# Performance work log

Measured on AMD Instinct MI355X. Metric: run time of the kernel, lower is better.

The kernel has to match this reference:

```python
import jax, jax.numpy as jnp
import numpy as np

DN = ('NCHW', 'OIHW', 'NCHW')

def conv2d(x, w, b, stride, pad):
    y = jax.lax.conv_general_dilated(x, w, (stride, stride), [(pad, pad), (pad, pad)], dimension_numbers=DN)
    return y + b[None, :, None, None]

def conv_transpose2d(x, w, b):
    # torch ConvTranspose2d(k=4, stride=2, padding=1): out = (H-1)*2 - 2 + 4 = 2H
    # implemented as input-dilated conv with padding k-1-p = 2 on each side
    y = jax.lax.conv_general_dilated(x, w, (1, 1), [(2, 2), (2, 2)], lhs_dilation=(2, 2), dimension_numbers=DN)
    return y + b[None, :, None, None]

def setup_inputs() -> dict:
    key = jax.random.key(0)
    ks = jax.random.split(key, 8)
    K, D = 512, 128
    x = jax.random.normal(ks[0], (32, 3, 128, 128), jnp.float32)
    ew1 = jax.random.normal(ks[1], (128, 3, 4, 4), jnp.float32) * (1.0 / np.sqrt(3 * 16))
    eb1 = jnp.zeros((128,), jnp.float32)
    ew2 = jax.random.normal(ks[2], (D, 128, 4, 4), jnp.float32) * (1.0 / np.sqrt(128 * 16))
    eb2 = jnp.zeros((D,), jnp.float32)
    E = jax.random.uniform(ks[3], (K, D), jnp.float32, minval=-1.0 / K, maxval=1.0 / K)
    dw1 = jax.random.normal(ks[4], (128, D, 4, 4), jnp.float32) * (1.0 / np.sqrt(D * 16))
    db1 = jnp.zeros((128,), jnp.float32)
    dw2 = jax.random.normal(ks[5], (3, 128, 4, 4), jnp.float32) * (1.0 / np.sqrt(128 * 16))
    db2 = jnp.zeros((3,), jnp.float32)
    return {"x": x, "ew1": ew1, "eb1": eb1, "ew2": ew2, "eb2": eb2, "E": E,
            "dw1": dw1, "db1": db1, "dw2": dw2, "db2": db2}

def reference(x, ew1, eb1, ew2, eb2, E, dw1, db1, dw2, db2):
    # --- encoder: conv stack ---
    h = jax.nn.relu(conv2d(x, ew1, eb1, stride=2, pad=1))       # [B,128,64,64]
    z = conv2d(h, ew2, eb2, stride=2, pad=1)                    # [B,D,32,32] encoder_output
    B, C, H, W = z.shape
    Ze = jnp.transpose(z, (0, 2, 3, 1)).reshape(-1, C)          # [N_e, D], BHWC flattening
    # --- VQ: pairwise sq-dist, argmin, codebook lookup (== one-hot matmul in original) ---
    d = (jnp.sum(Ze * Ze, axis=1, keepdims=True)
         + jnp.sum(E * E, axis=1)
         - 2.0 * jnp.matmul(Ze, E.T))                           # [N_e, K]
    idx = jnp.argmin(d, axis=1)                                 # [N_e]
    Zq = E[idx]                                                 # [N_e, D]
    # faithful to original: Zq_mat.view(encoder_output.shape) with NO permute back
    dec_in = Zq.reshape(B, C, H, W)
    # straight-through estimator
    dec_in = z + jax.lax.stop_gradient(dec_in - z)
    # --- decoder: transposed conv stack ---
    g = jax.nn.relu(conv_transpose2d(dec_in, dw1, db1))         # [B,128,64,64]
    x_recon = jax.nn.sigmoid(conv_transpose2d(g, dw2, db2))     # [B,3,128,128]
    return x_recon
```

## Files before the change

kernel.cpp:

```cpp
#include <hip/hip_runtime.h>
#include <hip/hip_bf16.h>
#include <math.h>


typedef __attribute__((ext_vector_type(8))) short bf16x8;
typedef __attribute__((ext_vector_type(4))) float f32x4;

__device__ __forceinline__ void gload16(const void* g, const void* l) {
    __builtin_amdgcn_global_load_lds(
        (const __attribute__((address_space(1))) void*)g,
        (__attribute__((address_space(3))) void*)l, 16, 0, 0);
}

__device__ __forceinline__ int fragoff(int row, int ks, int lane) {
    return (row << 8) + (((ks << 6) + (lane & 0x30)) ^ ((row & 7) << 4));
}
__device__ __forceinline__ int fragoff64(int row, int ks, int lane) {
    return (row << 7) + (((ks << 6) + (lane & 0x30)) ^ ((row & 7) << 4));
}

__global__ __launch_bounds__(256) void k_init(
    const float* __restrict__ ew1, const float* __restrict__ ew2,
    const float* __restrict__ E,   const float* __restrict__ dw1,
    const float* __restrict__ dw2,
    __hip_bfloat16* __restrict__ hb,  __hip_bfloat16* __restrict__ w2s,
    __hip_bfloat16* __restrict__ w1s, __hip_bfloat16* __restrict__ Eb,
    __hip_bfloat16* __restrict__ w1b, __hip_bfloat16* __restrict__ w2db9,
    __hip_bfloat16* __restrict__ dq,  float* __restrict__ s2)
{
    int bid = blockIdx.x, t = threadIdx.x;
    if (bid < 4160) {
        int tid = bid * 256 + t;
        const int NROW = 32 * 2 * 66 * 128;
        if (tid < NROW) {
            int c = tid & 127;
            int xx = (tid >> 7) % 66;
            int r2 = tid / (66 * 128);
            int yy = (r2 & 1) * 65;
            int n = r2 >> 1;
            hb[((n * 66 + yy) * 66 + xx) * 128 + c] = __float2bfloat16(0.f);
        } else {
            int t2 = tid - NROW;
            int c = t2 & 127;
            int xs = (t2 >> 7) & 1;
            int yy = ((t2 >> 8) & 63) + 1;
            int n = t2 >> 14;
            hb[((n * 66 + yy) * 66 + xs * 65) * 128 + c] = __float2bfloat16(0.f);
        }
    } else if (bid < 5184) {
        int tid = (bid - 4160) * 256 + t;
        int cpos = tid & 127, o = (tid >> 7) & 127, rs = tid >> 14;
        int r = rs >> 2, s = rs & 3;
        int slot = cpos >> 3, e = cpos & 7;
        int csrc = ((slot ^ (o & 7)) << 3) | e;
        w2s[tid] = __float2bfloat16(ew2[((o * 128 + csrc) * 4 + r) * 4 + s]);
    } else if (bid < 6208) {
        int tid = (bid - 5184) * 256 + t;
        int cpos = tid & 127, o = (tid >> 7) & 127, m = tid >> 14;
        int pe = (m >> 3) & 1, qe = (m >> 2) & 1, tt = (m >> 1) & 1, u = m & 1;
        int slot = cpos >> 3, e = cpos & 7;
        int csrc = ((slot ^ (o & 7)) << 3) | e;
        w1s[tid] = __float2bfloat16(dw1[((o * 128 + csrc) * 4 + (pe + 2 * tt)) * 4 + (qe + 2 * u)]);
    } else if (bid < 6464) {
        int tid = (bid - 6208) * 256 + t;
        int cpos = tid & 127, k = tid >> 7;
        int slot = cpos >> 3, e = cpos & 7;
        int csrc = ((slot ^ (k & 7)) << 3) | e;
        Eb[tid] = __float2bfloat16(E[k * 128 + csrc]);
    } else if (bid < 6496) {
        int tid = (bid - 6464) * 256 + t;
        int o = tid >> 6, cpos = tid & 63;
        int slot = cpos >> 3, e = cpos & 7;
        int k = ((slot ^ (o & 7)) << 3) | e;
        float v = 0.f;
        if (k < 48) {
            int c = k >> 4, r = (k >> 2) & 3, s = k & 3;
            v = ew1[((o * 3 + c) * 4 + r) * 4 + s];
        }
        w1b[tid] = __float2bfloat16(v);
    } else if (bid < 6568) {
        int tid = (bid - 6496) * 256 + t;
        int cpos = tid & 127;
        int col = (tid >> 7) & 15;
        int de = tid >> 11;
        int o = col & 3, pq = col >> 2;
        int d = de / 3, e_ = de - d * 3;
        int pe = pq >> 1, qe = pq & 1;
        int tt = d - pe, u = e_ - qe;
        float v = 0.f;
        if (o < 3 && tt >= 0 && tt < 2 && u >= 0 && u < 2) {
            int slot = cpos >> 3, el = cpos & 7;
            int csrc = ((slot ^ (col & 7)) << 3) | el;
            v = dw2[((o * 128 + csrc) * 4 + (pe + 2 * tt)) * 4 + (qe + 2 * u)];
        }
        w2db9[tid] = __float2bfloat16(v);
    } else if (bid < 6570) {
        int k = (bid - 6568) * 256 + t;
        float a = 0.f;
        const float* e = E + k * 128;
        for (int c = 0; c < 128; ++c) a = fmaf(e[c], e[c], a);
        s2[k] = a;
    } else {
        int tid = (bid - 6570) * 256 + t;
        int n = tid / 16896;
        int rem = tid - n * 16896;
        int c = rem & 127;
        int pp = rem >> 7;
        int yy, xx;
        if (pp < 68) { yy = (pp >= 34) ? 33 : 0; xx = pp % 34; }
        else { int q = pp - 68; yy = 1 + (q >> 1); xx = (q & 1) * 33; }
        dq[((n * 34 + yy) * 34 + xx) * 128 + c] = __float2bfloat16(0.f);
    }
}

__global__ __launch_bounds__(256) void k_conv1g(
    const float* __restrict__ x, const __hip_bfloat16* __restrict__ w1b,
    const float* __restrict__ b1, __hip_bfloat16* __restrict__ hb)
{
    __shared__ char smem[32768];
    int t = threadIdx.x, lane = t & 63, w = t >> 6;
    int wr = w >> 1, wc = w & 1;
    int bid0 = blockIdx.x;
    int bid = ((bid0 & 7) << 7) | (bid0 >> 3);
    int posbase = bid << 7;

    #pragma unroll
    for (int i = 0; i < 4; ++i)
        gload16(w1b + ((w * 4 + i) * 512 + lane * 8), &smem[16384 + ((w * 4 + i) << 10)]);

    {
        int row = t >> 1, half = t & 1;
        int rowg = posbase + row;
        int n = rowg >> 12, p = (rowg >> 6) & 63, q = rowg & 63;
        #pragma unroll
        for (int j = 0; j < 4; ++j) {
            int d = half * 4 + j;
            int sct = d ^ (row & 7);
            __hip_bfloat16 hv[8];
            #pragma unroll
            for (int e = 0; e < 8; ++e) {
                int k = sct * 8 + e;
                float v = 0.f;
                if (k < 48) {
                    int c = k >> 4, r = (k >> 2) & 3, s4 = k & 3;
                    int y = 2 * p + r - 1, xx = 2 * q + s4 - 1;
                    if (((unsigned)y < 128u) && ((unsigned)xx < 128u))
                        v = x[((n * 3 + c) * 128 + y) * 128 + xx];
                }
                hv[e] = __float2bfloat16(v);
            }
            *(bf16x8*)&smem[(row << 7) + d * 16] = *(bf16x8*)hv;
        }
    }
    __syncthreads();

    f32x4 acc[4][4];
    #pragma unroll
    for (int mi = 0; mi < 4; ++mi)
        #pragma unroll
        for (int ni = 0; ni < 4; ++ni) acc[mi][ni] = (f32x4){0.f, 0.f, 0.f, 0.f};

    #pragma unroll
    for (int ks = 0; ks < 2; ++ks) {
        bf16x8 av[4], bv[4];
        #pragma unroll
        for (int mi = 0; mi < 4; ++mi)
            av[mi] = *(const bf16x8*)&smem[fragoff64((wr << 6) + (mi << 4) + (lane & 15), ks, lane)];
        #pragma unroll
        for (int ni = 0; ni < 4; ++ni)
            bv[ni] = *(const bf16x8*)&smem[16384 + fragoff64((wc << 6) + (ni << 4) + (lane & 15), ks, lane)];
        #pragma unroll
        for (int mi = 0; mi < 4; ++mi)
            #pragma unroll
            for (int ni = 0; ni < 4; ++ni)
                acc[mi][ni] = __builtin_amdgcn_mfma_f32_16x16x32_bf16(av[mi], bv[ni], acc[mi][ni], 0, 0, 0);
    }

    int rg = (lane >> 4) << 2;
    #pragma unroll
    for (int mi = 0; mi < 4; ++mi)
        #pragma unroll
        for (int ni = 0; ni < 4; ++ni) {
            int o = (wc << 6) + (ni << 4) + (lane & 15);
            float bias = b1[o];
            #pragma unroll
            for (int j = 0; j < 4; ++j) {
                int rowg = posbase + (wr << 6) + (mi << 4) + rg + j;
                int n = rowg >> 12, p = (rowg >> 6) & 63, q = rowg & 63;
                float v = acc[mi][ni][j] + bias;
                v = v > 0.f ? v : 0.f;
                hb[((n * 66 + p + 1) * 66 + q + 1) * 128 + o] = __float2bfloat16(v);
            }
        }
}

__global__ __launch_bounds__(256) void k_conv2(
    const __hip_bfloat16* __restrict__ hb, const __hip_bfloat16* __restrict__ w2s,
    const float* __restrict__ b2, __hip_bfloat16* __restrict__ zb)
{
    __shared__ char smem[49152];
    int t = threadIdx.x, lane = t & 63, w = t >> 6;
    int bid0 = blockIdx.x;
    int bid = ((bid0 & 7) << 6) | (bid0 >> 3);
    int posbase = bid << 6;
    int n = posbase >> 10, p0 = (posbase >> 5) & 31;

    int aoff[4];
    #pragma unroll
    for (int i = 0; i < 4; ++i) {
        int row = (((w << 2) + i) << 2) + (lane >> 4);
        int slot = lane & 15;
        int p = p0 + (row >> 5), q = row & 31;
        int csw = (slot ^ (row & 7)) << 3;
        aoff[i] = (((n * 66 + 2 * p) * 66 + 2 * q) << 7) + csw;
    }

    f32x4 acc[4][2];
    #pragma unroll
    for (int mi = 0; mi < 4; ++mi)
        #pragma unroll
        for (int ni = 0; ni < 2; ++ni) acc[mi][ni] = (f32x4){0.f, 0.f, 0.f, 0.f};

    for (int rs = 0; rs < 16; ++rs) {
        __syncthreads();
        int rsoff = (((rs >> 2) * 66 + (rs & 3)) << 7);
        const __hip_bfloat16* wsl = w2s + (rs << 14);
        #pragma unroll
        for (int i = 0; i < 4; ++i)
            gload16(hb + aoff[i] + rsoff, &smem[((w << 2) + i) << 10]);
        #pragma unroll
        for (int i = 0; i < 8; ++i)
            gload16(wsl + ((((w << 3) + i) << 9) + (lane << 3)), &smem[16384 + (((w << 3) + i) << 10)]);
        __syncthreads();
        #pragma unroll
        for (int ks = 0; ks < 4; ++ks) {
            bf16x8 av[4], bv[2];
            #pragma unroll
            for (int mi = 0; mi < 4; ++mi)
                av[mi] = *(const bf16x8*)&smem[fragoff((mi << 4) + (lane & 15), ks, lane)];
            #pragma unroll
            for (int ni = 0; ni < 2; ++ni)
                bv[ni] = *(const bf16x8*)&smem[16384 + fragoff((w << 5) + (ni << 4) + (lane & 15), ks, lane)];
            #pragma unroll
            for (int mi = 0; mi < 4; ++mi)
                #pragma unroll
                for (int ni = 0; ni < 2; ++ni)
                    acc[mi][ni] = __builtin_amdgcn_mfma_f32_16x16x32_bf16(av[mi], bv[ni], acc[mi][ni], 0, 0, 0);
        }
    }

    int rg = (lane >> 4) << 2;
    #pragma unroll
    for (int mi = 0; mi < 4; ++mi)
        #pragma unroll
        for (int ni = 0; ni < 2; ++ni) {
            int o = (w << 5) + (ni << 4) + (lane & 15);
            float bias = b2[o];
            #pragma unroll
            for (int j = 0; j < 4; ++j) {
                int pos = posbase + (mi << 4) + rg + j;
                zb[(pos << 7) + o] = __float2bfloat16(acc[mi][ni][j] + bias);
            }
        }
}

__global__ __launch_bounds__(256) void k_vq(
    const __hip_bfloat16* __restrict__ zb, const __hip_bfloat16* __restrict__ Eb,
    const float* __restrict__ s2, const float* __restrict__ E,
    __hip_bfloat16* __restrict__ dq)
{
    __shared__ char smem[65536];
    int t = threadIdx.x, lane = t & 63, w = t >> 6;
    int wr = w >> 1, wc = w & 1;
    int posbase = blockIdx.x << 7;

    #pragma unroll
    for (int i = 0; i < 8; ++i) {
        int row = (((w << 3) + i) << 2) + (lane >> 4);
        int slot = lane & 15;
        int csw = (slot ^ (row & 7)) << 3;
        gload16(zb + (((posbase + row) << 7) + csw), &smem[((w << 3) + i) << 10]);
    }

    float bvv[4][4];
    int   bii[4][4];
    #pragma unroll
    for (int mi = 0; mi < 4; ++mi)
        #pragma unroll
        for (int j = 0; j < 4; ++j) { bvv[mi][j] = 3.4e38f; bii[mi][j] = 0; }

    for (int n0 = 0; n0 < 4; ++n0) {
        __syncthreads();
        const __hip_bfloat16* esl = Eb + (n0 << 14);
        #pragma unroll
        for (int i = 0; i < 8; ++i)
            gload16(esl + ((((w << 3) + i) << 9) + (lane << 3)), &smem[32768 + (((w << 3) + i) << 10)]);
        __syncthreads();

        f32x4 acc[4][4];
        #pragma unroll
        for (int mi = 0; mi < 4; ++mi)
            #pragma unroll
            for (int ni = 0; ni < 4; ++ni) acc[mi][ni] = (f32x4){0.f, 0.f, 0.f, 0.f};

        #pragma unroll
        for (int ks = 0; ks < 4; ++ks) {
            bf16x8 av[4], bv[4];
            #pragma unroll
            for (int mi = 0; mi < 4; ++mi)
                av[mi] = *(const bf16x8*)&smem[fragoff((wr << 6) + (mi << 4) + (lane & 15), ks, lane)];
            #pragma unroll
            for (int ni = 0; ni < 4; ++ni)
                bv[ni] = *(const bf16x8*)&smem[32768 + fragoff((wc << 6) + (ni << 4) + (lane & 15), ks, lane)];
            #pragma unroll
            for (int mi = 0; mi < 4; ++mi)
                #pragma unroll
                for (int ni = 0; ni < 4; ++ni)
                    acc[mi][ni] = __builtin_amdgcn_mfma_f32_16x16x32_bf16(av[mi], bv[ni], acc[mi][ni], 0, 0, 0);
        }

        float s2v[4];
        #pragma unroll
        for (int ni = 0; ni < 4; ++ni)
            s2v[ni] = s2[(n0 << 7) + (wc << 6) + (ni << 4) + (lane & 15)];
        #pragma unroll
        for (int mi = 0; mi < 4; ++mi)
            #pragma unroll
            for (int ni = 0; ni < 4; ++ni) {
                int k = (n0 << 7) + (wc << 6) + (ni << 4) + (lane & 15);
                #pragma unroll
                for (int j = 0; j < 4; ++j) {
                    float sc = s2v[ni] - 2.f * acc[mi][ni][j];
                    if (sc < bvv[mi][j]) { bvv[mi][j] = sc; bii[mi][j] = k; }
                }
            }
    }

    __syncthreads();
    float* redv  = (float*)smem;
    int*   redi  = (int*)(smem + 1024);
    int*   idx_l = (int*)(smem + 32768);
    #pragma unroll
    for (int mi = 0; mi < 4; ++mi)
        #pragma unroll
        for (int j = 0; j < 4; ++j) {
            float v = bvv[mi][j];
            int   ix = bii[mi][j];
            #pragma unroll
            for (int m = 1; m < 16; m <<= 1) {
                float ov = __shfl_xor(v, m, 64);
                int   oi = __shfl_xor(ix, m, 64);
                if (ov < v || (ov == v && oi < ix)) { v = ov; ix = oi; }
            }
            if ((lane & 15) == 0) {
                int row = (wr << 6) + (mi << 4) + ((lane >> 4) << 2) + j;
                redv[row * 2 + wc] = v;
                redi[row * 2 + wc] = ix;
            }
        }
    __syncthreads();
    if (t < 128) {
        float v0 = redv[t * 2], v1 = redv[t * 2 + 1];
        int   i0 = redi[t * 2], i1 = redi[t * 2 + 1];
        idx_l[t] = (v1 < v0 || (v1 == v0 && i1 < i0)) ? i1 : i0;
    }
    __syncthreads();

    {
        int j = t >> 1, half = t & 1;
        const float* er = E + idx_l[j] * 128 + half * 64;
        unsigned short* dstl = (unsigned short*)smem + j * 128 + half * 64;
        #pragma unroll
        for (int q4 = 0; q4 < 16; ++q4) {
            float4 v = *(const float4*)(er + q4 * 4);
            union { __hip_bfloat16 h[4]; unsigned long long u; } pk;
            pk.h[0] = __float2bfloat16(v.x); pk.h[1] = __float2bfloat16(v.y);
            pk.h[2] = __float2bfloat16(v.z); pk.h[3] = __float2bfloat16(v.w);
            *(unsigned long long*)(dstl + q4 * 4) = pk.u;
        }
    }
    __syncthreads();

    int n = posbase >> 10;
    int cb = (posbase >> 3) & 127;
    const unsigned short* eb = (const unsigned short*)smem;
    #pragma unroll
    for (int k2 = 0; k2 < 4; ++k2) {
        int sp = k2 * 256 + t;
        int hi = sp >> 7, lo = sp & 127;
        int y = hi * 4 + (lo >> 5), x = lo & 31;
        unsigned short vals[16];
        #pragma unroll
        for (int ci = 0; ci < 16; ++ci)
            vals[ci] = eb[((((ci << 3) | hi)) << 7) + lo];
        __hip_bfloat16* dst = dq + ((n * 34 + y + 1) * 34 + (x + 1)) * 128 + cb;
        *(bf16x8*)dst = *(bf16x8*)&vals[0];
        *(bf16x8*)(dst + 8) = *(bf16x8*)&vals[8];
    }
}

__global__ __launch_bounds__(256) void k_deconv1(
    const __hip_bfloat16* __restrict__ dq, const __hip_bfloat16* __restrict__ w1s,
    const float* __restrict__ b1, __hip_bfloat16* __restrict__ g)
{
    __shared__ char smem[65536];
    int t = threadIdx.x, lane = t & 63, w = t >> 6;
    int wr = w >> 1, wc = w & 1;
    int bid0 = blockIdx.x;
    int bid = ((bid0 & 7) << 7) | (bid0 >> 3);
    int ag = bid & 7, qe = (bid >> 3) & 1, pe = (bid >> 4) & 1, n = bid >> 5;

    int aoff[8];
    #pragma unroll
    for (int i = 0; i < 8; ++i) {
        int row = (((w << 3) + i) << 2) + (lane >> 4);
        int slot = lane & 15;
        int a = (ag << 2) + (row >> 5), b = row & 31;
        int csw = (slot ^ (row & 7)) << 3;
        aoff[i] = (((n * 34 + (a + pe)) * 34 + (b + qe)) << 7) + csw;
    }

    f32x4 acc[4][4];
    #pragma unroll
    for (int mi = 0; mi < 4; ++mi)
        #pragma unroll
        for (int ni = 0; ni < 4; ++ni) acc[mi][ni] = (f32x4){0.f, 0.f, 0.f, 0.f};

    for (int tu = 0; tu < 4; ++tu) {
        __syncthreads();
        int tt = tu >> 1, u = tu & 1;
        int tapoff = ((tt * 34 + u) << 7);
        const __hip_bfloat16* wsl = w1s + ((((pe << 3) | (qe << 2) | tu)) << 14);
        #pragma unroll
        for (int i = 0; i < 8; ++i) {
            gload16(dq + aoff[i] + tapoff, &smem[((w << 3) + i) << 10]);
            gload16(wsl + ((((w << 3) + i) << 9) + (lane << 3)), &smem[32768 + (((w << 3) + i) << 10)]);
        }
        __syncthreads();
        #pragma unroll
        for (int ks = 0; ks < 4; ++ks) {
            bf16x8 av[4], bv[4];
            #pragma unroll
            for (int mi = 0; mi < 4; ++mi)
                av[mi] = *(const bf16x8*)&smem[fragoff((wr << 6) + (mi << 4) + (lane & 15), ks, lane)];
            #pragma unroll
            for (int ni = 0; ni < 4; ++ni)
                bv[ni] = *(const bf16x8*)&smem[32768 + fragoff((wc << 6) + (ni << 4) + (lane & 15), ks, lane)];
            #pragma unroll
            for (int mi = 0; mi < 4; ++mi)
                #pragma unroll
                for (int ni = 0; ni < 4; ++ni)
                    acc[mi][ni] = __builtin_amdgcn_mfma_f32_16x16x32_bf16(av[mi], bv[ni], acc[mi][ni], 0, 0, 0);
        }
    }

    int rg = (lane >> 4) << 2;
    #pragma unroll
    for (int mi = 0; mi < 4; ++mi)
        #pragma unroll
        for (int ni = 0; ni < 4; ++ni) {
            int o = (wc << 6) + (ni << 4) + (lane & 15);
            float bias = b1[o];
            #pragma unroll
            for (int j = 0; j < 4; ++j) {
                int row = (wr << 6) + (mi << 4) + rg + j;
                int a = (ag << 2) + (row >> 5), b = row & 31;
                int y = 2 * a + pe, xx2 = 2 * b + qe;
                float v = acc[mi][ni][j] + bias;
                v = v > 0.f ? v : 0.f;
                g[((n * 66 + y + 1) * 66 + xx2 + 1) * 128 + o] = __float2bfloat16(v);
            }
        }
}

__global__ __launch_bounds__(256) void k_deconv2g(
    const __hip_bfloat16* __restrict__ g, const __hip_bfloat16* __restrict__ w2db9,
    const float* __restrict__ b2, float* __restrict__ out)
{
    __shared__ char smem[36864];
    int t = threadIdx.x, lane = t & 63, w = t >> 6;
    int bid0 = blockIdx.x;
    int bid = ((bid0 & 7) << 7) | (bid0 >> 3);
    int atile = bid & 31, n = bid >> 5;
    int a0 = atile << 1;

    int aoff[8];
    #pragma unroll
    for (int i = 0; i < 8; ++i) {
        int row = (((w << 3) + i) << 2) + (lane >> 4);
        int al = row >> 6, b = row & 63;
        int csw = ((lane & 15) ^ (row & 7)) << 3;
        aoff[i] = (((n * 66 + (a0 + al)) * 66 + b) << 7) + csw;
    }

    f32x4 acc[2];
    acc[0] = (f32x4){0.f, 0.f, 0.f, 0.f};
    acc[1] = (f32x4){0.f, 0.f, 0.f, 0.f};

    for (int de = 0; de < 9; ++de) {
        __syncthreads();
        int dy = de / 3, dx = de - dy * 3;
        int tapoff = ((dy * 66 + dx) << 7);
        #pragma unroll
        for (int i = 0; i < 8; ++i)
            gload16(g + aoff[i] + tapoff, &smem[((w << 3) + i) << 10]);
        gload16(w2db9 + (de << 11) + (w << 9) + (lane << 3), &smem[32768 + (w << 10)]);
        __syncthreads();
        #pragma unroll
        for (int ks = 0; ks < 4; ++ks) {
            bf16x8 av[2], bv;
            #pragma unroll
            for (int mi = 0; mi < 2; ++mi)
                av[mi] = *(const bf16x8*)&smem[fragoff((w << 5) + (mi << 4) + (lane & 15), ks, lane)];
            bv = *(const bf16x8*)&smem[32768 + fragoff(lane & 15, ks, lane)];
            #pragma unroll
            for (int mi = 0; mi < 2; ++mi)
                acc[mi] = __builtin_amdgcn_mfma_f32_16x16x32_bf16(av[mi], bv, acc[mi], 0, 0, 0);
        }
    }

    int rg = (lane >> 4) << 2;
    int col = lane & 15, o = col & 3, pq = col >> 2;
    if (o < 3) {
        int pe = pq >> 1, qe = pq & 1;
        float bias = b2[o];
        #pragma unroll
        for (int mi = 0; mi < 2; ++mi)
            #pragma unroll
            for (int j = 0; j < 4; ++j) {
                int row = (w << 5) + (mi << 4) + rg + j;
                int y = 2 * (a0 + (row >> 6)) + pe;
                int x = 2 * (row & 63) + qe;
                float v = acc[mi][j] + bias;
                out[((n * 3 + o) * 128 + y) * 128 + x] = 1.f / (1.f + expf(-v));
            }
    }
}

extern "C" void kernel_launch(void* const* d_in, const int* in_sizes, int n_in,
                              void* d_out, int out_size, void* d_ws, size_t ws_size,
                              hipStream_t stream) {
    const float* x   = (const float*)d_in[0];
    const float* ew1 = (const float*)d_in[1];
    const float* eb1 = (const float*)d_in[2];
    const float* ew2 = (const float*)d_in[3];
    const float* eb2 = (const float*)d_in[4];
    const float* E   = (const float*)d_in[5];
    const float* dw1 = (const float*)d_in[6];
    const float* db1 = (const float*)d_in[7];
    const float* dw2 = (const float*)d_in[8];
    const float* db2 = (const float*)d_in[9];
    float* out = (float*)d_out;

    char* W = (char*)d_ws;
    __hip_bfloat16* hb    = (__hip_bfloat16*)(W + 0);
    __hip_bfloat16* g     = (__hip_bfloat16*)(W + 0);
    __hip_bfloat16* zb    = (__hip_bfloat16*)(W + 67108864);
    __hip_bfloat16* dq    = (__hip_bfloat16*)(W + 75497472);
    __hip_bfloat16* w2s   = (__hip_bfloat16*)(W + 84967424);
    __hip_bfloat16* w1s   = (__hip_bfloat16*)(W + 85491712);
    __hip_bfloat16* Eb    = (__hip_bfloat16*)(W + 86016000);
    __hip_bfloat16* w2db9 = (__hip_bfloat16*)(W + 86147072);
    float*          s2    = (float*)(W + 86184192);
    __hip_bfloat16* w1b   = (__hip_bfloat16*)(W + 86186240);

    k_init    <<<8682,  256, 0, stream>>>(ew1, ew2, E, dw1, dw2,
                                          hb, w2s, w1s, Eb, w1b, w2db9, dq, s2);
    k_conv1g  <<<1024,  256, 0, stream>>>(x, w1b, eb1, hb);
    k_conv2   <<<512,   256, 0, stream>>>(hb, w2s, eb2, zb);
    k_vq      <<<256,   256, 0, stream>>>(zb, Eb, s2, E, dq);
    k_deconv1 <<<1024,  256, 0, stream>>>(dq, w1s, db1, g);
    k_deconv2g<<<1024,  256, 0, stream>>>(g, w2db9, db2, out);
}
```

Measured before the change: 119.8 us.

## Fuse encoder conv2 with VQ argmin and halve LDS tiles via K-chunking

Merges the second encoder conv and the vector-quantization kernel into one kernel. The conv output tile stays in LDS as bf16 and is matched against codebook chunks directly, so the zb intermediate is neither written to nor read back from global memory, and one launch is removed. Codebook rows are now gathered as bf16 from the prepared table instead of converting fp32 E rows. Weights are stored unswizzled, and the conv2 and deconv1 K loops are split into two 64-channel chunks per tap, cutting LDS to 32KB to allow more resident blocks. The cost is twice as many barrier-separated load steps and a VQ that now works on 64 rows per block instead of 128.

```diff
diff --git a/kernel.cpp b/kernel.cpp
--- a/kernel.cpp
+++ b/kernel.cpp
@@ -23,8 +23,8 @@
     const float* __restrict__ ew1, const float* __restrict__ ew2,
     const float* __restrict__ E,   const float* __restrict__ dw1,
     const float* __restrict__ dw2,
-    __hip_bfloat16* __restrict__ hb,  __hip_bfloat16* __restrict__ w2s,
-    __hip_bfloat16* __restrict__ w1s, __hip_bfloat16* __restrict__ Eb,
+    __hip_bfloat16* __restrict__ hb,  __hip_bfloat16* __restrict__ w2p,
+    __hip_bfloat16* __restrict__ w1p, __hip_bfloat16* __restrict__ Ep,
     __hip_bfloat16* __restrict__ w1b, __hip_bfloat16* __restrict__ w2db9,
     __hip_bfloat16* __restrict__ dq,  float* __restrict__ s2)
 {
@@ -49,24 +49,17 @@
         }
     } else if (bid < 5184) {
         int tid = (bid - 4160) * 256 + t;
-        int cpos = tid & 127, o = (tid >> 7) & 127, rs = tid >> 14;
+        int c = tid & 127, o = (tid >> 7) & 127, rs = tid >> 14;
         int r = rs >> 2, s = rs & 3;
-        int slot = cpos >> 3, e = cpos & 7;
-        int csrc = ((slot ^ (o & 7)) << 3) | e;
-        w2s[tid] = __float2bfloat16(ew2[((o * 128 + csrc) * 4 + r) * 4 + s]);
+        w2p[tid] = __float2bfloat16(ew2[((o * 128 + c) * 4 + r) * 4 + s]);
     } else if (bid < 6208) {
         int tid = (bid - 5184) * 256 + t;
-        int cpos = tid & 127, o = (tid >> 7) & 127, m = tid >> 14;
+        int c = tid & 127, o = (tid >> 7) & 127, m = tid >> 14;
         int pe = (m >> 3) & 1, qe = (m >> 2) & 1, tt = (m >> 1) & 1, u = m & 1;
-        int slot = cpos >> 3, e = cpos & 7;
-        int csrc = ((slot ^ (o & 7)) << 3) | e;
-        w1s[tid] = __float2bfloat16(dw1[((o * 128 + csrc) * 4 + (pe + 2 * tt)) * 4 + (qe + 2 * u)]);
+        w1p[tid] = __float2bfloat16(dw1[((o * 128 + c) * 4 + (pe + 2 * tt)) * 4 + (qe + 2 * u)]);
     } else if (bid < 6464) {
         int tid = (bid - 6208) * 256 + t;
-        int cpos = tid & 127, k = tid >> 7;
-        int slot = cpos >> 3, e = cpos & 7;
-        int csrc = ((slot ^ (k & 7)) << 3) | e;
-        Eb[tid] = __float2bfloat16(E[k * 128 + csrc]);
+        Ep[tid] = __float2bfloat16(E[tid]);
     } else if (bid < 6496) {
         int tid = (bid - 6464) * 256 + t;
         int o = tid >> 6, cpos = tid & 63;
@@ -194,25 +187,32 @@
         }
 }
 
-__global__ __launch_bounds__(256) void k_conv2(
-    const __hip_bfloat16* __restrict__ hb, const __hip_bfloat16* __restrict__ w2s,
-    const float* __restrict__ b2, __hip_bfloat16* __restrict__ zb)
+__global__ __launch_bounds__(256) void k_conv2vq(
+    const __hip_bfloat16* __restrict__ hb, const __hip_bfloat16* __restrict__ w2p,
+    const float* __restrict__ b2, const __hip_bfloat16* __restrict__ Ep,
+    const float* __restrict__ s2, __hip_bfloat16* __restrict__ dq)
 {
-    __shared__ char smem[49152];
+    __shared__ char smem[32768];
     int t = threadIdx.x, lane = t & 63, w = t >> 6;
     int bid0 = blockIdx.x;
     int bid = ((bid0 & 7) << 6) | (bid0 >> 3);
     int posbase = bid << 6;
     int n = posbase >> 10, p0 = (posbase >> 5) & 31;
 
-    int aoff[4];
+    int aoff[2];
+    #pragma unroll
+    for (int i = 0; i < 2; ++i) {
+        int r = ((w << 1) + i) * 8 + (lane >> 3);
+        int slot = lane & 7;
+        int p = p0 + (r >> 5), q = r & 31;
+        aoff[i] = (((n * 66 + 2 * p) * 66 + 2 * q) << 7) + ((slot ^ (r & 7)) << 3);
+    }
+    int boff[4];
     #pragma unroll
     for (int i = 0; i < 4; ++i) {
-        int row = (((w << 2) + i) << 2) + (lane >> 4);
-        int slot = lane & 15;
-        int p = p0 + (row >> 5), q = row & 31;
-        int csw = (slot ^ (row & 7)) << 3;
-        aoff[i] = (((n * 66 + 2 * p) * 66 + 2 * q) << 7) + csw;
+        int o = ((w << 2) + i) * 8 + (lane >> 3);
+        int slot = lane & 7;
+        boff[i] = (o << 7) + ((slot ^ (o & 7)) << 3);
     }
 
     f32x4 acc[4][2];
@@ -221,26 +221,27 @@
         #pragma unroll
         for (int ni = 0; ni < 2; ++ni) acc[mi][ni] = (f32x4){0.f, 0.f, 0.f, 0.f};
 
-    for (int rs = 0; rs < 16; ++rs) {
-        __syncthreads();
-        int rsoff = (((rs >> 2) * 66 + (rs & 3)) << 7);
-        const __hip_bfloat16* wsl = w2s + (rs << 14);
+    for (int step = 0; step < 32; ++step) {
+        int rs = step >> 1, ch = step & 1;
+        int aadd = ((((rs >> 2) * 66) + (rs & 3)) << 7) + (ch << 6);
+        int badd = (rs << 14) + (ch << 6);
+        __syncthreads();
+        #pragma unroll
+        for (int i = 0; i < 2; ++i)
+            gload16(hb + aoff[i] + aadd, &smem[((w << 1) + i) << 10]);
         #pragma unroll
         for (int i = 0; i < 4; ++i)
-            gload16(hb + aoff[i] + rsoff, &smem[((w << 2) + i) << 10]);
-        #pragma unroll
-        for (int i = 0; i < 8; ++i)
-            gload16(wsl + ((((w << 3) + i) << 9) + (lane << 3)), &smem[16384 + (((w << 3) + i) << 10)]);
-        __syncthreads();
-        #pragma unroll
-        for (int ks = 0; ks < 4; ++ks) {
+            gload16(w2p + boff[i] + badd, &smem[16384 + (((w << 2) + i) << 10)]);
+        __syncthreads();
+        #pragma unroll
+        for (int ks = 0; ks < 2; ++ks) {
             bf16x8 av[4], bv[2];
             #pragma unroll
             for (int mi = 0; mi < 4; ++mi)
-                av[mi] = *(const bf16x8*)&smem[fragoff((mi << 4) + (lane & 15), ks, lane)];
+                av[mi] = *(const bf16x8*)&smem[fragoff64((mi << 4) + (lane & 15), ks, lane)];
             #pragma unroll
             for (int ni = 0; ni < 2; ++ni)
-                bv[ni] = *(const bf16x8*)&smem[16384 + fragoff((w << 5) + (ni << 4) + (lane & 15), ks, lane)];
+                bv[ni] = *(const bf16x8*)&smem[16384 + fragoff64((w << 5) + (ni << 4) + (lane & 15), ks, lane)];
             #pragma unroll
             for (int mi = 0; mi < 4; ++mi)
                 #pragma unroll
@@ -249,38 +250,25 @@
         }
     }
 
-    int rg = (lane >> 4) << 2;
-    #pragma unroll
-    for (int mi = 0; mi < 4; ++mi)
-        #pragma unroll
-        for (int ni = 0; ni < 2; ++ni) {
-            int o = (w << 5) + (ni << 4) + (lane & 15);
-            float bias = b2[o];
-            #pragma unroll
-            for (int j = 0; j < 4; ++j) {
-                int pos = posbase + (mi << 4) + rg + j;
-                zb[(pos << 7) + o] = __float2bfloat16(acc[mi][ni][j] + bias);
-            }
-        }
-}
-
-__global__ __launch_bounds__(256) void k_vq(
-    const __hip_bfloat16* __restrict__ zb, const __hip_bfloat16* __restrict__ Eb,
-    const float* __restrict__ s2, const float* __restrict__ E,
-    __hip_bfloat16* __restrict__ dq)
-{
-    __shared__ char smem[65536];
-    int t = threadIdx.x, lane = t & 63, w = t >> 6;
-    int wr = w >> 1, wc = w & 1;
-    int posbase = blockIdx.x << 7;
-
-    #pragma unroll
-    for (int i = 0; i < 8; ++i) {
-        int row = (((w << 3) + i) << 2) + (lane >> 4);
-        int slot = lane & 15;
-        int csw = (slot ^ (row & 7)) << 3;
-        gload16(zb + (((posbase + row) << 7) + csw), &smem[((w << 3) + i) << 10]);
-    }
+    __syncthreads();
+    {
+        int rg = (lane >> 4) << 2;
+        #pragma unroll
+        for (int mi = 0; mi < 4; ++mi)
+            #pragma unroll
+            for (int ni = 0; ni < 2; ++ni) {
+                int o = (w << 5) + (ni << 4) + (lane & 15);
+                float bias = b2[o];
+                #pragma unroll
+                for (int j = 0; j < 4; ++j) {
+                    int r = (mi << 4) + rg + j;
+                    int byteoff = (r << 8) + (((((o >> 3) ^ (r & 7))) << 4) | ((o & 7) << 1));
+                    __hip_bfloat16 hv = __float2bfloat16(acc[mi][ni][j] + bias);
+                    *(__hip_bfloat16*)&smem[byteoff] = hv;
+                }
+            }
+    }
+    __syncthreads();
 
     float bvv[4][4];
     int   bii[4][4];
@@ -289,57 +277,45 @@
         #pragma unroll
         for (int j = 0; j < 4; ++j) { bvv[mi][j] = 3.4e38f; bii[mi][j] = 0; }
 
-    for (int n0 = 0; n0 < 4; ++n0) {
-        __syncthreads();
-        const __hip_bfloat16* esl = Eb + (n0 << 14);
-        #pragma unroll
-        for (int i = 0; i < 8; ++i)
-            gload16(esl + ((((w << 3) + i) << 9) + (lane << 3)), &smem[32768 + (((w << 3) + i) << 10)]);
-        __syncthreads();
-
-        f32x4 acc[4][4];
+    for (int chunk = 0; chunk < 8; ++chunk) {
+        __syncthreads();
+        #pragma unroll
+        for (int i = 0; i < 4; ++i) {
+            int kl = (((w << 2) + i) << 2) + (lane >> 4);
+            int slot = lane & 15;
+            gload16(Ep + ((((chunk << 6) + kl) << 7) + ((slot ^ (kl & 7)) << 3)),
+                    &smem[16384 + (((w << 2) + i) << 10)]);
+        }
+        __syncthreads();
+        f32x4 a2[4];
+        #pragma unroll
+        for (int mi = 0; mi < 4; ++mi) a2[mi] = (f32x4){0.f, 0.f, 0.f, 0.f};
+        #pragma unroll
+        for (int ks = 0; ks < 4; ++ks) {
+            bf16x8 av[4], bv;
+            #pragma unroll
+            for (int mi = 0; mi < 4; ++mi)
+                av[mi] = *(const bf16x8*)&smem[fragoff((mi << 4) + (lane & 15), ks, lane)];
+            bv = *(const bf16x8*)&smem[16384 + fragoff((w << 4) + (lane & 15), ks, lane)];
+            #pragma unroll
+            for (int mi = 0; mi < 4; ++mi)
+                a2[mi] = __builtin_amdgcn_mfma_f32_16x16x32_bf16(av[mi], bv, a2[mi], 0, 0, 0);
+        }
+        int kg = (chunk << 6) + (w << 4) + (lane & 15);
+        float s2v = s2[kg];
         #pragma unroll
         for (int mi = 0; mi < 4; ++mi)
             #pragma unroll
-            for (int ni = 0; ni < 4; ++ni) acc[mi][ni] = (f32x4){0.f, 0.f, 0.f, 0.f};
-
-        #pragma unroll
-        for (int ks = 0; ks < 4; ++ks) {
-            bf16x8 av[4], bv[4];
-            #pragma unroll
-            for (int mi = 0; mi < 4; ++mi)
-                av[mi] = *(const bf16x8*)&smem[fragoff((wr << 6) + (mi << 4) + (lane & 15), ks, lane)];
-            #pragma unroll
-            for (int ni = 0; ni < 4; ++ni)
-                bv[ni] = *(const bf16x8*)&smem[32768 + fragoff((wc << 6) + (ni << 4) + (lane & 15), ks, lane)];
-            #pragma unroll
-            for (int mi = 0; mi < 4; ++mi)
-                #pragma unroll
-                for (int ni = 0; ni < 4; ++ni)
-                    acc[mi][ni] = __builtin_amdgcn_mfma_f32_16x16x32_bf16(av[mi], bv[ni], acc[mi][ni], 0, 0, 0);
-        }
-
-        float s2v[4];
-        #pragma unroll
-        for (int ni = 0; ni < 4; ++ni)
-            s2v[ni] = s2[(n0 << 7) + (wc << 6) + (ni << 4) + (lane & 15)];
-        #pragma unroll
-        for (int mi = 0; mi < 4; ++mi)
-            #pragma unroll
-            for (int ni = 0; ni < 4; ++ni) {
-                int k = (n0 << 7) + (wc << 6) + (ni << 4) + (lane & 15);
-                #pragma unroll
-                for (int j = 0; j < 4; ++j) {
-                    float sc = s2v[ni] - 2.f * acc[mi][ni][j];
-                    if (sc < bvv[mi][j]) { bvv[mi][j] = sc; bii[mi][j] = k; }
-                }
-            }
-    }
-
-    __syncthreads();
-    float* redv  = (float*)smem;
-    int*   redi  = (int*)(smem + 1024);
-    int*   idx_l = (int*)(smem + 32768);
+            for (int j = 0; j < 4; ++j) {
+                float sc = s2v - 2.f * a2[mi][j];
+                if (sc < bvv[mi][j]) { bvv[mi][j] = sc; bii[mi][j] = kg; }
+            }
+    }
+
+    __syncthreads();
+    float* redv  = (float*)&smem[16384];
+    int*   redi  = (int*)&smem[16384 + 1024];
+    int*   idx_l = (int*)&smem[16384 + 2048];
     #pragma unroll
     for (int mi = 0; mi < 4; ++mi)
         #pragma unroll
@@ -353,71 +329,69 @@
                 if (ov < v || (ov == v && oi < ix)) { v = ov; ix = oi; }
             }
             if ((lane & 15) == 0) {
-                int row = (wr << 6) + (mi << 4) + ((lane >> 4) << 2) + j;
-                redv[row * 2 + wc] = v;
-                redi[row * 2 + wc] = ix;
-            }
-        }
-    __syncthreads();
-    if (t < 128) {
-        float v0 = redv[t * 2], v1 = redv[t * 2 + 1];
-        int   i0 = redi[t * 2], i1 = redi[t * 2 + 1];
-        idx_l[t] = (v1 < v0 || (v1 == v0 && i1 < i0)) ? i1 : i0;
-    }
-    __syncthreads();
-
-    {
-        int j = t >> 1, half = t & 1;
-        const float* er = E + idx_l[j] * 128 + half * 64;
-        unsigned short* dstl = (unsigned short*)smem + j * 128 + half * 64;
-        #pragma unroll
-        for (int q4 = 0; q4 < 16; ++q4) {
-            float4 v = *(const float4*)(er + q4 * 4);
-            union { __hip_bfloat16 h[4]; unsigned long long u; } pk;
-            pk.h[0] = __float2bfloat16(v.x); pk.h[1] = __float2bfloat16(v.y);
-            pk.h[2] = __float2bfloat16(v.z); pk.h[3] = __float2bfloat16(v.w);
-            *(unsigned long long*)(dstl + q4 * 4) = pk.u;
-        }
-    }
-    __syncthreads();
-
-    int n = posbase >> 10;
-    int cb = (posbase >> 3) & 127;
+                int r = (mi << 4) + ((lane >> 4) << 2) + j;
+                redv[(r << 2) + w] = v;
+                redi[(r << 2) + w] = ix;
+            }
+        }
+    __syncthreads();
+    if (t < 64) {
+        float bv_ = redv[t << 2];
+        int   bi_ = redi[t << 2];
+        #pragma unroll
+        for (int w2 = 1; w2 < 4; ++w2) {
+            float ov = redv[(t << 2) + w2];
+            int   oi = redi[(t << 2) + w2];
+            if (ov < bv_ || (ov == bv_ && oi < bi_)) { bv_ = ov; bi_ = oi; }
+        }
+        idx_l[t] = bi_;
+    }
+    __syncthreads();
+
+    #pragma unroll
+    for (int i = 0; i < 4; ++i) {
+        int idx2 = (w << 2) + i;
+        int r = (idx2 << 2) + (lane >> 4);
+        int krow = idx_l[r];
+        gload16(Ep + ((krow << 7) + ((lane & 15) << 3)), &smem[idx2 << 10]);
+    }
+    __syncthreads();
+
+    int cd0 = (posbase >> 3) & 127;
     const unsigned short* eb = (const unsigned short*)smem;
     #pragma unroll
     for (int k2 = 0; k2 < 4; ++k2) {
-        int sp = k2 * 256 + t;
+        int sp = (k2 << 8) + t;
         int hi = sp >> 7, lo = sp & 127;
-        int y = hi * 4 + (lo >> 5), x = lo & 31;
-        unsigned short vals[16];
-        #pragma unroll
-        for (int ci = 0; ci < 16; ++ci)
-            vals[ci] = eb[((((ci << 3) | hi)) << 7) + lo];
-        __hip_bfloat16* dst = dq + ((n * 34 + y + 1) * 34 + (x + 1)) * 128 + cb;
-        *(bf16x8*)dst = *(bf16x8*)&vals[0];
-        *(bf16x8*)(dst + 8) = *(bf16x8*)&vals[8];
+        int y = sp >> 5, xx = sp & 31;
+        unsigned short vals[8];
+        #pragma unroll
+        for (int ci = 0; ci < 8; ++ci)
+            vals[ci] = eb[(((ci << 3) + hi) << 7) + lo];
+        __hip_bfloat16* dst = dq + ((n * 34 + y + 1) * 34 + (xx + 1)) * 128 + cd0;
+        *(bf16x8*)dst = *(bf16x8*)vals;
     }
 }
 
 __global__ __launch_bounds__(256) void k_deconv1(
-    const __hip_bfloat16* __restrict__ dq, const __hip_bfloat16* __restrict__ w1s,
+    const __hip_bfloat16* __restrict__ dq, const __hip_bfloat16* __restrict__ w1p,
     const float* __restrict__ b1, __hip_bfloat16* __restrict__ g)
 {
-    __shared__ char smem[65536];
+    __shared__ char smem[32768];
     int t = threadIdx.x, lane = t & 63, w = t >> 6;
     int wr = w >> 1, wc = w & 1;
     int bid0 = blockIdx.x;
     int bid = ((bid0 & 7) << 7) | (bid0 >> 3);
     int ag = bid & 7, qe = (bid >> 3) & 1, pe = (bid >> 4) & 1, n = bid >> 5;
 
-    int aoff[8];
-    #pragma unroll
-    for (int i = 0; i < 8; ++i) {
-        int row = (((w << 3) + i) << 2) + (lane >> 4);
-        int slot = lane & 15;
-        int a = (ag << 2) + (row >> 5), b = row & 31;
-        int csw = (slot ^ (row & 7)) << 3;
-        aoff[i] = (((n * 34 + (a + pe)) * 34 + (b + qe)) << 7) + csw;
+    int aoff[4], boff[4];
+    #pragma unroll
+    for (int i = 0; i < 4; ++i) {
+        int r = ((w << 2) + i) * 8 + (lane >> 3);
+        int slot = lane & 7;
+        int a = (ag << 2) + (r >> 5), b = r & 31;
+        aoff[i] = (((n * 34 + (a + pe)) * 34 + (b + qe)) << 7) + ((slot ^ (r & 7)) << 3);
+        boff[i] = (r << 7) + ((slot ^ (r & 7)) << 3);
     }
 
     f32x4 acc[4][4];
@@ -426,26 +400,28 @@
         #pragma unroll
         for (int ni = 0; ni < 4; ++ni) acc[mi][ni] = (f32x4){0.f, 0.f, 0.f, 0.f};
 
-    for (int tu = 0; tu < 4; ++tu) {
-        __syncthreads();
+    int mbase = (pe << 3) | (qe << 2);
+    for (int step = 0; step < 8; ++step) {
+        int tu = step >> 1, ch = step & 1;
         int tt = tu >> 1, u = tu & 1;
-        int tapoff = ((tt * 34 + u) << 7);
-        const __hip_bfloat16* wsl = w1s + ((((pe << 3) | (qe << 2) | tu)) << 14);
-        #pragma unroll
-        for (int i = 0; i < 8; ++i) {
-            gload16(dq + aoff[i] + tapoff, &smem[((w << 3) + i) << 10]);
-            gload16(wsl + ((((w << 3) + i) << 9) + (lane << 3)), &smem[32768 + (((w << 3) + i) << 10)]);
-        }
-        __syncthreads();
-        #pragma unroll
-        for (int ks = 0; ks < 4; ++ks) {
+        int aadd = ((tt * 34 + u) << 7) + (ch << 6);
+        int badd = ((mbase + tu) << 14) + (ch << 6);
+        __syncthreads();
+        #pragma unroll
+        for (int i = 0; i < 4; ++i) {
+            gload16(dq + aoff[i] + aadd, &smem[((w << 2) + i) << 10]);
+            gload16(w1p + boff[i] + badd, &smem[16384 + (((w << 2) + i) << 10)]);
+        }
+        __syncthreads();
+        #pragma unroll
+        for (int ks = 0; ks < 2; ++ks) {
             bf16x8 av[4], bv[4];
             #pragma unroll
             for (int mi = 0; mi < 4; ++mi)
-                av[mi] = *(const bf16x8*)&smem[fragoff((wr << 6) + (mi << 4) + (lane & 15), ks, lane)];
+                av[mi] = *(const bf16x8*)&smem[fragoff64((wr << 6) + (mi << 4) + (lane & 15), ks, lane)];
             #pragma unroll
             for (int ni = 0; ni < 4; ++ni)
-                bv[ni] = *(const bf16x8*)&smem[32768 + fragoff((wc << 6) + (ni << 4) + (lane & 15), ks, lane)];
+                bv[ni] = *(const bf16x8*)&smem[16384 + fragoff64((wc << 6) + (ni << 4) + (lane & 15), ks, lane)];
             #pragma unroll
             for (int mi = 0; mi < 4; ++mi)
                 #pragma unroll
@@ -555,20 +531,18 @@
     char* W = (char*)d_ws;
     __hip_bfloat16* hb    = (__hip_bfloat16*)(W + 0);
     __hip_bfloat16* g     = (__hip_bfloat16*)(W + 0);
-    __hip_bfloat16* zb    = (__hip_bfloat16*)(W + 67108864);
     __hip_bfloat16* dq    = (__hip_bfloat16*)(W + 75497472);
-    __hip_bfloat16* w2s   = (__hip_bfloat16*)(W + 84967424);
-    __hip_bfloat16* w1s   = (__hip_bfloat16*)(W + 85491712);
-    __hip_bfloat16* Eb    = (__hip_bfloat16*)(W + 86016000);
+    __hip_bfloat16* w2p   = (__hip_bfloat16*)(W + 84967424);
+    __hip_bfloat16* w1p   = (__hip_bfloat16*)(W + 85491712);
+    __hip_bfloat16* Ep    = (__hip_bfloat16*)(W + 86016000);
     __hip_bfloat16* w2db9 = (__hip_bfloat16*)(W + 86147072);
     float*          s2    = (float*)(W + 86184192);
     __hip_bfloat16* w1b   = (__hip_bfloat16*)(W + 86186240);
 
-    k_init    <<<8682,  256, 0, stream>>>(ew1, ew2, E, dw1, dw2,
-                                          hb, w2s, w1s, Eb, w1b, w2db9, dq, s2);
-    k_conv1g  <<<1024,  256, 0, stream>>>(x, w1b, eb1, hb);
-    k_conv2   <<<512,   256, 0, stream>>>(hb, w2s, eb2, zb);
-    k_vq      <<<256,   256, 0, stream>>>(zb, Eb, s2, E, dq);
-    k_deconv1 <<<1024,  256, 0, stream>>>(dq, w1s, db1, g);
-    k_deconv2g<<<1024,  256, 0, stream>>>(g, w2db9, db2, out);
-}
+    k_init    <<<8682, 256, 0, stream>>>(ew1, ew2, E, dw1, dw2,
+                                         hb, w2p, w1p, Ep, w1b, w2db9, dq, s2);
+    k_conv1g  <<<1024, 256, 0, stream>>>(x, w1b, eb1, hb);
+    k_conv2vq <<<512,  256, 0, stream>>>(hb, w2p, eb2, Ep, s2, dq);
+    k_deconv1 <<<1024, 256, 0, stream>>>(dq, w1p, db1, g);
+    k_deconv2g<<<1024, 256, 0, stream>>>(g, w2db9, db2, out);
+}
```

Result: no change. 119.7 us (-0.1%).
